# Optimization experiments

Hardware: AMD Instinct MI355X
Metric: run time of the kernel (lower is better)

## Reference

```python
import jax, jax.numpy as jnp
import numpy as np

N_NODES = 10000
N_EDGES = 160000
C_IN = 64      # in_irreps = 64x0e
C_TP = 16      # in_tp_irreps = 16x0e
C_KEY = 8      # key_irreps = (mul//2) = 8x0e
C_SH = 4       # spherical_harmonics_irreps = 4x0e
C_OTP = 16     # out_tp_irreps = 16x0e
C_OUT = 64     # out_irreps = 64x0e
EF = 32        # n_edge_features
FC = 128       # fc_dim (hardcoded in module)
W_NUMEL_K = C_TP * C_SH * C_KEY   # 512
W_NUMEL_V = C_TP * C_SH * C_OTP   # 1024
EPS = 1e-5


def _mlp(x, W1, b1, W2, b2, W3, b3):
    h = jax.nn.relu(x @ W1 + b1)
    h = jax.nn.relu(h @ W2 + b2)
    return h @ W3 + b3


def setup_inputs() -> dict:
    key = jax.random.key(0)
    ks = jax.random.split(key, 24)
    def nrm(k, shape, scale=1.0):
        return jax.random.normal(k, shape, dtype=jnp.float32) * scale
    inp = {}
    inp["node_data"] = nrm(ks[0], (N_NODES, C_IN))
    inp["edge_index"] = jax.random.randint(ks[1], (2, N_EDGES), 0, N_NODES, dtype=jnp.int32)
    inp["edge_data"] = nrm(ks[2], (N_EDGES, EF))
    inp["edge_sh"] = nrm(ks[3], (N_EDGES, C_SH))
    # e3nn Linear / TP internal weights (scalar-irrep specialization)
    inp["W_input"] = nrm(ks[4], (C_IN, C_TP))
    inp["W_query"] = nrm(ks[5], (C_TP, C_KEY))
    inp["W_dot"] = nrm(ks[6], (C_KEY, C_KEY))
    inp["W_output"] = nrm(ks[7], (C_OTP, C_OUT))
    # fc_key MLP: EF -> FC -> FC -> W_NUMEL_K
    inp["Wk1"] = nrm(ks[8], (EF, FC), 1.0 / np.sqrt(EF)); inp["bk1"] = jnp.zeros((FC,), jnp.float32)
    inp["Wk2"] = nrm(ks[9], (FC, FC), 1.0 / np.sqrt(FC)); inp["bk2"] = jnp.zeros((FC,), jnp.float32)
    inp["Wk3"] = nrm(ks[10], (FC, W_NUMEL_K), 1.0 / np.sqrt(FC)); inp["bk3"] = jnp.zeros((W_NUMEL_K,), jnp.float32)
    # fc_value MLP: EF -> FC -> FC -> W_NUMEL_V
    inp["Wv1"] = nrm(ks[11], (EF, FC), 1.0 / np.sqrt(EF)); inp["bv1"] = jnp.zeros((FC,), jnp.float32)
    inp["Wv2"] = nrm(ks[12], (FC, FC), 1.0 / np.sqrt(FC)); inp["bv2"] = jnp.zeros((FC,), jnp.float32)
    inp["Wv3"] = nrm(ks[13], (FC, W_NUMEL_V), 1.0 / np.sqrt(FC)); inp["bv3"] = jnp.zeros((W_NUMEL_V,), jnp.float32)
    inp["bn_weight"] = jnp.ones((C_OUT,), jnp.float32)
    inp["bn_bias"] = jnp.zeros((C_OUT,), jnp.float32)
    return inp


def reference(node_data, edge_index, edge_data, edge_sh,
              W_input, W_query, W_dot, W_output,
              Wk1, bk1, Wk2, bk2, Wk3, bk3,
              Wv1, bv1, Wv2, bv2, Wv3, bv3,
              bn_weight, bn_bias):
    N = node_data.shape[0]
    E = edge_data.shape[0]
    src, dst = edge_index[0], edge_index[1]

    # input_linear (e3nn Linear -> fan-in normalized matmul for scalar irreps)
    t = node_data @ W_input / np.sqrt(C_IN)          # [N, C_TP]
    q = t @ W_query / np.sqrt(C_TP)                  # [N, C_KEY]

    # dynamically generated per-edge TP weights
    wk = _mlp(edge_data, Wk1, bk1, Wk2, bk2, Wk3, bk3).reshape(E, C_TP, C_SH, C_KEY)
    wv = _mlp(edge_data, Wv1, bv1, Wv2, bv2, Wv3, bv3).reshape(E, C_TP, C_SH, C_OTP)

    ts = t[src]                                      # gather source node features [E, C_TP]
    # FullyConnectedTensorProduct on scalar irreps == per-edge weighted bilinear
    k = jnp.einsum('ea,es,easb->eb', ts, edge_sh, wk) / np.sqrt(C_TP * C_SH)   # [E, C_KEY]
    v = jnp.einsum('ea,es,easb->eb', ts, edge_sh, wv) / np.sqrt(C_TP * C_SH)   # [E, C_OTP]

    # dot(q[dest], k) -> scalar attention logit per edge
    a = (jnp.einsum('ea,eb,ab->e', q[dst], k, W_dot) / np.sqrt(C_KEY * C_KEY))[:, None]  # [E, 1]

    # segment softmax over edges grouped by destination node
    m = jax.ops.segment_max(a, dst, num_segments=N)
    m = jnp.where(jnp.isfinite(m), m, 0.0)           # empty segments -> 0 (matches scatter_max fill)
    a = jnp.exp(a - m[dst])
    z = jax.ops.segment_sum(a, dst, num_segments=N)
    a = a / z[dst]

    agg = jax.ops.segment_sum(a * v, dst, num_segments=N)   # [N, C_OTP]

    out = agg @ W_output / np.sqrt(C_OTP)            # [N, C_OUT]
    # residual: F.pad(node_data, (0, C_OUT - C_IN)); here C_OUT == C_IN so plain add
    out = out + node_data

    # e3nn BatchNorm on scalar irreps (training-mode batch stats, affine)
    mean = out.mean(axis=0)
    c = out - mean
    var = (c * c).mean(axis=0)
    out = c * jax.lax.rsqrt(var + EPS) * bn_weight + bn_bias
    return out
```

## Files before the change

kernel.cpp:

```cpp
#include <hip/hip_runtime.h>

#define N_NODES 10000
#define N_EDGES 160000

typedef unsigned short u16;
typedef unsigned int   u32;
typedef __bf16 bf16x8 __attribute__((ext_vector_type(8)));
typedef float  f32x4  __attribute__((ext_vector_type(4)));
typedef unsigned short u16x4 __attribute__((ext_vector_type(4)));

struct InP { const void* p[22]; };

static constexpr size_t WS_FLAG = 0;
static constexpr size_t WS_WIN  = 256;
static constexpr size_t WS_WQ   = WS_WIN  + 4096;
static constexpr size_t WS_WD   = WS_WQ   + 512;
static constexpr size_t WS_WOUT = WS_WD   + 256;
static constexpr size_t WS_BK1  = WS_WOUT + 4096;
static constexpr size_t WS_BK2  = WS_BK1  + 512;
static constexpr size_t WS_BK3  = WS_BK2  + 512;
static constexpr size_t WS_BV1  = WS_BK3  + 2048;
static constexpr size_t WS_BV2  = WS_BV1  + 512;
static constexpr size_t WS_BV3  = WS_BV2  + 512;
static constexpr size_t WS_BNW  = WS_BV3  + 4096;
static constexpr size_t WS_BNB  = WS_BNW  + 256;
static constexpr size_t WS_WK1T = WS_BNB  + 256;
static constexpr size_t WS_WK2T = WS_WK1T + 8192;
static constexpr size_t WS_WK3T = WS_WK2T + 32768;
static constexpr size_t WS_WV1T = WS_WK3T + 131072;
static constexpr size_t WS_WV2T = WS_WV1T + 8192;
static constexpr size_t WS_WV3T = WS_WV2T + 32768;
static constexpr size_t WS_T    = WS_WV3T + 262144;
static constexpr size_t WS_Q    = WS_T    + (size_t)N_NODES*16*4;
static constexpr size_t WS_Z    = WS_Q    + (size_t)N_NODES*8*4;
static constexpr size_t WS_AGG  = WS_Z    + (size_t)N_NODES*4;
static constexpr size_t WS_BNS  = WS_AGG  + (size_t)N_NODES*16*4;
static constexpr size_t WS_BNQ  = WS_BNS  + 256;
static constexpr size_t WS_OUTP = WS_BNQ  + 256;
static constexpr size_t ZERO_OFF = WS_Z;
static constexpr size_t ZERO_LEN = WS_OUTP - WS_Z;

__device__ __forceinline__ float loadf(const void* p, long i, int isbf){
  if(isbf){
    u32 x = ((u32)((const u16*)p)[i]) << 16;
    return __uint_as_float(x);
  }
  return ((const float*)p)[i];
}
__device__ __forceinline__ u16 f2b(float f){
  u32 u = __float_as_uint(f);
  u += 0x7fffu + ((u >> 16) & 1u);
  return (u16)(u >> 16);
}
__device__ __forceinline__ float b2f(u16 v){
  return __uint_as_float(((u32)v) << 16);
}
__device__ __forceinline__ bf16x8 ld8(const u16* p){
  uint4 v = *(const uint4*)p;
  return __builtin_bit_cast(bf16x8, v);
}

__global__ void k_detect(const void* edge_data, int* flag){
  int lane = threadIdx.x;
  u16 v = ((const u16*)edge_data)[lane*2];
  int ex = (v >> 7) & 0xFF;
  int sane = (ex >= 100 && ex <= 140) ? 1 : 0;
  unsigned long long b = __ballot(sane);
  if(lane == 0) flag[0] = (__popcll(b) >= 48) ? 1 : 0;
}

__global__ void k_convert(InP in, char* ws){
  const int isbf = *(const int*)(ws + WS_FLAG);
  long idx = (long)blockIdx.x*256 + threadIdx.x;
  const int    fsrc[12] = {4,5,6,7,9,11,13,15,17,19,20,21};
  const int    fcnt[12] = {1024,128,64,1024,128,128,512,128,128,1024,64,64};
  const size_t fdst[12] = {WS_WIN,WS_WQ,WS_WD,WS_WOUT,WS_BK1,WS_BK2,WS_BK3,WS_BV1,WS_BV2,WS_BV3,WS_BNW,WS_BNB};
  const long F_TOTAL = 4416;
  if(idx < F_TOTAL){
    long g = idx;
    for(int s=0;s<12;s++){
      if(g < fcnt[s]){ ((float*)(ws+fdst[s]))[g] = loadf(in.p[fsrc[s]], g, isbf); return; }
      g -= fcnt[s];
    }
    return;
  }
  long g = idx - F_TOTAL;
  const int    tsrc[6] = {8,10,12,14,16,18};
  const int    tK[6]   = {32,128,128,32,128,128};
  const int    tN[6]   = {128,128,512,128,128,1024};
  const size_t tdst[6] = {WS_WK1T,WS_WK2T,WS_WK3T,WS_WV1T,WS_WV2T,WS_WV3T};
  for(int s=0;s<6;s++){
    long cnt = (long)tK[s]*tN[s];
    if(g < cnt){
      int nk = tK[s] >> 5;
      int i = (int)(g & 7), ln = (int)((g>>3) & 63);
      int r2 = (int)(g >> 9);
      int kk = r2 % nk; int r3 = r2 / nk;
      int nt = r3 & 1;  int c  = r3 >> 1;
      int n = c*32 + nt*16 + (ln & 15);
      int k = kk*32 + (ln >> 4)*8 + i;
      ((u16*)(ws+tdst[s]))[g] = f2b(loadf(in.p[tsrc[s]], (long)k*tN[s] + n, isbf));
      return;
    }
    g -= cnt;
  }
}

__global__ void k_tq(InP in, char* ws){
  const int isbf = *(const int*)(ws + WS_FLAG);
  __shared__ float sWin[1024];
  __shared__ float sWq[128];
  __shared__ float sN[1024];
  __shared__ float sT[256];
  float* t_ws = (float*)(ws+WS_T);
  float* q_ws = (float*)(ws+WS_Q);
  int tid = threadIdx.x;
  for(int i=tid;i<1024;i+=256) sWin[i] = ((const float*)(ws+WS_WIN))[i];
  if(tid<128) sWq[tid] = ((const float*)(ws+WS_WQ))[tid];
  int n0 = blockIdx.x*16;
  for(int i=tid;i<1024;i+=256) sN[i] = loadf(in.p[0], (long)n0*64 + i, isbf);
  __syncthreads();
  int ni = tid>>4, j = tid&15;
  float acc = 0.f;
  #pragma unroll 8
  for(int i=0;i<64;i++) acc += sN[ni*64+i]*sWin[i*16+j];
  float t = acc*0.125f;
  t_ws[(n0+ni)*16+j] = t;
  sT[tid] = t;
  __syncthreads();
  if(tid<128){
    int n2 = tid>>3, b = tid&7;
    float a2 = 0.f;
    #pragma unroll
    for(int jj=0;jj<16;jj++) a2 += sT[n2*16+jj]*sWq[jj*8+b];
    q_ws[(n0+n2)*8+b] = a2*0.25f;
  }
}

__global__ __launch_bounds__(256,3) void k_edges(InP in, char* ws){
  const int isbf = *(const int*)(ws + WS_FLAG);
  const int* ei = (const int*)in.p[1];
  const float* t_ws = (const float*)(ws + WS_T);
  const float* q_ws = (const float*)(ws + WS_Q);
  float* Zp  = (float*)(ws + WS_Z);
  float* AGG = (float*)(ws + WS_AGG);

  __shared__ __align__(16) char smem[51200];
  u16*   sED = (u16*)smem;
  u16*   sH1 = (u16*)(smem + 4096);
  u16*   sH2 = (u16*)(smem + 20480);
  u16*   sPT = (u16*)(smem + 36864);
  float* sK  = (float*)(smem + 45056);
  float* sV  = (float*)(smem + 47104);
  float* sP  = (float*)smem;
  int*   sDst= (int*)(smem + 256);

  const int tid  = threadIdx.x;
  const int e0   = blockIdx.x * 64;
  const int lane = tid & 63, wv = tid >> 6;
  const int lrow = lane & 15, lquad = lane >> 4;

  {
    int e = tid >> 2, q4 = tid & 3;
    u16 tmp[8];
    if(isbf){
      uint4 vv = *(const uint4*)((const u16*)in.p[2] + (long)(e0+e)*32 + q4*8);
      *(uint4*)tmp = vv;
    } else {
      const float* fp = (const float*)in.p[2] + (long)(e0+e)*32 + q4*8;
      f32x4 a = *(const f32x4*)fp, b = *(const f32x4*)(fp+4);
      #pragma unroll
      for(int r=0;r<4;r++){ tmp[r]=f2b(a[r]); tmp[4+r]=f2b(b[r]); }
    }
    *(uint4*)&sED[(e>>4)*512 + (q4*16 + (e&15))*8] = *(uint4*)tmp;
  }
  {
    int e = tid >> 2, j4 = tid & 3;
    int src = ei[e0+e];
    *(f32x4*)&sV[e*16 + j4*4] = *(const f32x4*)&t_ws[src*16 + j4*4];
  }
  {
    int e = tid >> 2, s4 = tid & 3;
    sK[tid] = loadf(in.p[3], (long)(e0+e)*4 + s4, isbf);
  }
  float qreg[8]; int mydst = 0;
  if(wv == 0){
    mydst = ei[N_EDGES + e0 + lane];
    #pragma unroll
    for(int a=0;a<8;a++) qreg[a] = q_ws[mydst*8 + a];
  }
  __syncthreads();
  for(int idx = tid; idx < 4096; idx += 256){
    int e = idx & 63, as = idx >> 6;
    sPT[as*64 + e] = f2b(sV[e*16 + (as>>2)] * sK[e*4 + (as&3)]);
  }
  __syncthreads();
  for(int idx = tid; idx < 1536; idx += 256) sK[idx] = 0.f;

  auto dense = [&](const u16* A, int ts, int nkL, const u16* Wg, const float* biasg, u16* O){
    bf16x8 bw[2][4]; f32x4 bb[2];
    for(int nt=0;nt<2;nt++){
      for(int kk=0;kk<nkL;kk++)
        bw[nt][kk] = ld8(&Wg[(((wv*2+nt)*nkL + kk)<<9) + lane*8]);
      bb[nt] = *(const f32x4*)&biasg[wv*32 + nt*16 + lquad*4];
    }
    for(int et=0;et<4;et++){
      bf16x8 af[4];
      for(int kk=0;kk<nkL;kk++) af[kk] = ld8(&A[et*ts + (kk<<9) + lane*8]);
      for(int nt=0;nt<2;nt++){
        f32x4 c = {0.f,0.f,0.f,0.f};
        for(int kk=0;kk<nkL;kk++)
          c = __builtin_amdgcn_mfma_f32_16x16x32_bf16(bw[nt][kk], af[kk], c, 0, 0, 0);
        u16x4 pk;
        #pragma unroll
        for(int r=0;r<4;r++){
          float h = c[r] + bb[nt][r];
          h = h > 0.f ? h : 0.f;
          pk[r] = f2b(h);
        }
        int off = et*2048 + (wv<<9) + (nt*2 + (lquad>>1))*128 + lrow*8 + (lquad&1)*4;
        *(u16x4*)&O[off] = pk;
      }
    }
  };

  auto matvec = [&](const u16* Wg, const float* biasg, int NJ, int isval){
    float kp[16];
    #pragma unroll
    for(int i=0;i<16;i++) kp[i]=0.f;
    const int c0 = wv*NJ;
    bf16x8 bw[2][2][4]; f32x4 bb[2][2];
    #pragma unroll
    for(int nt=0;nt<2;nt++){
      #pragma unroll
      for(int kk=0;kk<4;kk++)
        bw[0][nt][kk] = ld8(&Wg[(((c0*2+nt)*4 + kk)<<9) + lane*8]);
      bb[0][nt] = *(const f32x4*)&biasg[c0*32 + nt*16 + lquad*4];
    }
    #pragma unroll
    for(int j=0;j<NJ;j++){
      int cur = j&1, nxt = cur^1;
      if(j+1 < NJ){
        int cn = c0 + j + 1;
        #pragma unroll
        for(int nt=0;nt<2;nt++){
          #pragma unroll
          for(int kk=0;kk<4;kk++)
            bw[nxt][nt][kk] = ld8(&Wg[(((cn*2+nt)*4 + kk)<<9) + lane*8]);
          bb[nxt][nt] = *(const f32x4*)&biasg[cn*32 + nt*16 + lquad*4];
        }
      }
      for(int et=0;et<4;et++){
        bf16x8 af[4];
        #pragma unroll
        for(int kk=0;kk<4;kk++)
          af[kk] = ld8(&sH2[et*2048 + (kk<<9) + lane*8]);
        const int e = et*16 + lrow;
        for(int nt=0;nt<2;nt++){
          f32x4 c = {0.f,0.f,0.f,0.f};
          #pragma unroll
          for(int kk=0;kk<4;kk++)
            c = __builtin_amdgcn_mfma_f32_16x16x32_bf16(bw[cur][nt][kk], af[kk], c, 0, 0, 0);
          int n0 = (c0+j)*32 + nt*16 + lquad*4;
          int as = isval ? (n0>>4) : (n0>>3);
          float pv = b2f(sPT[as*64 + e]);
          #pragma unroll
          for(int r=0;r<4;r++)
            kp[et*4+r] += pv * (c[r] + bb[cur][nt][r]);
        }
      }
    }
    if(isval){
      for(int et=0;et<4;et++){
        int e = et*16 + lrow;
        #pragma unroll
        for(int r=0;r<4;r++)
          atomicAdd(&sV[e*16 + lquad*4 + r], kp[et*4+r]*0.125f);
      }
    } else {
      int b0 = (lquad & 1)*4;
      for(int et=0;et<4;et++){
        int e = et*16 + lrow;
        #pragma unroll
        for(int r=0;r<4;r++)
          atomicAdd(&sK[e*8 + b0 + r], kp[et*4+r]*0.125f);
      }
    }
  };

  dense(sED, 512, 1, (const u16*)(ws+WS_WK1T), (const float*)(ws+WS_BK1), sH1); __syncthreads();
  dense(sH1, 2048,4, (const u16*)(ws+WS_WK2T), (const float*)(ws+WS_BK2), sH2); __syncthreads();
  matvec((const u16*)(ws+WS_WK3T), (const float*)(ws+WS_BK3), 4, 0);
  dense(sED, 512, 1, (const u16*)(ws+WS_WV1T), (const float*)(ws+WS_BV1), sH1); __syncthreads();
  dense(sH1, 2048,4, (const u16*)(ws+WS_WV2T), (const float*)(ws+WS_BV2), sH2); __syncthreads();
  matvec((const u16*)(ws+WS_WV3T), (const float*)(ws+WS_BV3), 8, 1);            __syncthreads();

  if(wv == 0){
    const float* wdf = (const float*)(ws + WS_WD);
    float acc = 0.f;
    #pragma unroll
    for(int a=0;a<8;a++){
      float qa = qreg[a];
      #pragma unroll
      for(int b=0;b<8;b++)
        acc += qa * wdf[a*8+b] * sK[lane*8+b];
    }
    float p = __expf(acc * 0.125f);
    atomicAdd(Zp + mydst, p);
    sP[lane] = p;
    sDst[lane] = mydst;
  }
  __syncthreads();
  for(int idx = tid; idx < 1024; idx += 256){
    int e = idx >> 4;
    atomicAdd(AGG + (long)sDst[e]*16 + (idx & 15), sP[e]*sV[idx]);
  }
}

__global__ void k7a(InP in, char* ws){
  const int isbf = *(const int*)(ws + WS_FLAG);
  __shared__ float sWo[1024];
  __shared__ float ls[256], lq[256];
  int tid = threadIdx.x;
  for(int i=tid;i<1024;i+=256) sWo[i] = ((const float*)(ws+WS_WOUT))[i];
  __syncthreads();
  const float* AGG = (const float*)(ws+WS_AGG);
  const float* Zp  = (const float*)(ws+WS_Z);
  float* OUTP = (float*)(ws+WS_OUTP);
  int c = tid & 63, r4 = tid >> 6;
  float s=0.f, q=0.f;
  for(int it=0; it<20; it++){
    int n = blockIdx.x*80 + it*4 + r4;
    float z = Zp[n];
    float inv = z > 0.f ? 0.25f/z : 0.f;
    const float* ag = AGG + (long)n*16;
    float acc = 0.f;
    #pragma unroll
    for(int j=0;j<16;j++) acc += ag[j]*sWo[j*64+c];
    float o = acc*inv + loadf(in.p[0], (long)n*64 + c, isbf);
    OUTP[(long)n*64+c] = o;
    s += o; q += o*o;
  }
  ls[tid]=s; lq[tid]=q;
  __syncthreads();
  if(tid < 64){
    float ss = ls[tid]+ls[tid+64]+ls[tid+128]+ls[tid+192];
    float qq = lq[tid]+lq[tid+64]+lq[tid+128]+lq[tid+192];
    atomicAdd((float*)(ws+WS_BNS)+tid, ss);
    atomicAdd((float*)(ws+WS_BNQ)+tid, qq);
  }
}

__global__ void k7c(char* ws, void* d_out){
  const int isbf = *(const int*)(ws + WS_FLAG);
  int idx = blockIdx.x*256 + threadIdx.x;
  if(idx >= N_NODES*64) return;
  int c = idx & 63;
  float s  = ((const float*)(ws+WS_BNS))[c];
  float qq = ((const float*)(ws+WS_BNQ))[c];
  float mean = s * (1.f/N_NODES);
  float var  = qq * (1.f/N_NODES) - mean*mean;
  float sc = rsqrtf(var + 1e-5f) * ((const float*)(ws+WS_BNW))[c];
  float val = (((const float*)(ws+WS_OUTP))[idx] - mean)*sc + ((const float*)(ws+WS_BNB))[c];
  if(isbf) ((u16*)d_out)[idx] = f2b(val);
  else     ((float*)d_out)[idx] = val;
}

extern "C" void kernel_launch(void* const* d_in, const int* in_sizes, int n_in,
                              void* d_out, int out_size, void* d_ws, size_t ws_size,
                              hipStream_t stream){
  InP in;
  for(int i=0;i<22;i++) in.p[i] = d_in[i];
  char* ws = (char*)d_ws;

  hipMemsetAsync(ws + ZERO_OFF, 0, ZERO_LEN, stream);
  k_detect<<<1,64,0,stream>>>((const void*)d_in[2], (int*)(ws+WS_FLAG));
  k_convert<<<946,256,0,stream>>>(in, ws);
  k_tq<<<625,256,0,stream>>>(in, ws);
  k_edges<<<2500,256,0,stream>>>(in, ws);
  k7a<<<125,256,0,stream>>>(in, ws);
  k7c<<<2500,256,0,stream>>>(ws, d_out);
}
```

Before: 321.9 us.

## Merge prep kernels, fold edge-weight contraction into MFMA epilogue, shrink LDS

The detect, convert and node-projection kernels become one preprocessing launch. Each kernel now detects bf16 inputs inline, and small vectors are read straight from the inputs. In the edge kernel, the per-edge tensor-product weights are no longer staged as a bf16 outer-product buffer. The third MLP layer's output is contracted with the ts/sh values directly in registers, with the weight columns permuted to match, and reduced across lanes with shuffles instead of shared-memory atomics. Shared memory shrinks so occupancy can rise to 4 blocks per CU, and the node-output kernel gets twice as many blocks. This adds more cross-lane shuffles and repeated detection work in every block, and the new weight permutation is a correctness risk.

```diff
diff --git a/kernel.cpp b/kernel.cpp
--- a/kernel.cpp
+++ b/kernel.cpp
@@ -11,26 +11,15 @@
 
 struct InP { const void* p[22]; };
 
-static constexpr size_t WS_FLAG = 0;
-static constexpr size_t WS_WIN  = 256;
-static constexpr size_t WS_WQ   = WS_WIN  + 4096;
-static constexpr size_t WS_WD   = WS_WQ   + 512;
-static constexpr size_t WS_WOUT = WS_WD   + 256;
-static constexpr size_t WS_BK1  = WS_WOUT + 4096;
-static constexpr size_t WS_BK2  = WS_BK1  + 512;
-static constexpr size_t WS_BK3  = WS_BK2  + 512;
-static constexpr size_t WS_BV1  = WS_BK3  + 2048;
-static constexpr size_t WS_BV2  = WS_BV1  + 512;
-static constexpr size_t WS_BV3  = WS_BV2  + 512;
-static constexpr size_t WS_BNW  = WS_BV3  + 4096;
-static constexpr size_t WS_BNB  = WS_BNW  + 256;
-static constexpr size_t WS_WK1T = WS_BNB  + 256;
+static constexpr size_t WS_WK1T = 0;
 static constexpr size_t WS_WK2T = WS_WK1T + 8192;
 static constexpr size_t WS_WK3T = WS_WK2T + 32768;
 static constexpr size_t WS_WV1T = WS_WK3T + 131072;
 static constexpr size_t WS_WV2T = WS_WV1T + 8192;
 static constexpr size_t WS_WV3T = WS_WV2T + 32768;
-static constexpr size_t WS_T    = WS_WV3T + 262144;
+static constexpr size_t WS_BK3P = WS_WV3T + 262144;
+static constexpr size_t WS_BV3P = WS_BK3P + 2048;
+static constexpr size_t WS_T    = WS_BV3P + 4096;
 static constexpr size_t WS_Q    = WS_T    + (size_t)N_NODES*16*4;
 static constexpr size_t WS_Z    = WS_Q    + (size_t)N_NODES*8*4;
 static constexpr size_t WS_AGG  = WS_Z    + (size_t)N_NODES*4;
@@ -40,6 +29,13 @@
 static constexpr size_t ZERO_OFF = WS_Z;
 static constexpr size_t ZERO_LEN = WS_OUTP - WS_Z;
 
+__device__ __forceinline__ int detect_isbf(const void* ed){
+  int lane = threadIdx.x & 63;
+  u16 v = ((const u16*)ed)[lane*2];
+  int ex = (v >> 7) & 0xFF;
+  unsigned long long b = __ballot(ex >= 100 && ex <= 140);
+  return __popcll(b) >= 48;
+}
 __device__ __forceinline__ float loadf(const void* p, long i, int isbf){
   if(isbf){
     u32 x = ((u32)((const u16*)p)[i]) << 16;
@@ -47,6 +43,16 @@
   }
   return ((const float*)p)[i];
 }
+__device__ __forceinline__ f32x4 loadf4(const void* p, long i, int isbf){
+  if(isbf){
+    u16x4 v = *(const u16x4*)((const u16*)p + i);
+    f32x4 r;
+    #pragma unroll
+    for(int k=0;k<4;k++) r[k] = __uint_as_float(((u32)v[k])<<16);
+    return r;
+  }
+  return *(const f32x4*)((const float*)p + i);
+}
 __device__ __forceinline__ u16 f2b(float f){
   u32 u = __float_as_uint(f);
   u += 0x7fffu + ((u >> 16) & 1u);
@@ -60,54 +66,48 @@
   return __builtin_bit_cast(bf16x8, v);
 }
 
-__global__ void k_detect(const void* edge_data, int* flag){
-  int lane = threadIdx.x;
-  u16 v = ((const u16*)edge_data)[lane*2];
-  int ex = (v >> 7) & 0xFF;
-  int sane = (ex >= 100 && ex <= 140) ? 1 : 0;
-  unsigned long long b = __ballot(sane);
-  if(lane == 0) flag[0] = (__popcll(b) >= 48) ? 1 : 0;
-}
-
-__global__ void k_convert(InP in, char* ws){
-  const int isbf = *(const int*)(ws + WS_FLAG);
-  long idx = (long)blockIdx.x*256 + threadIdx.x;
-  const int    fsrc[12] = {4,5,6,7,9,11,13,15,17,19,20,21};
-  const int    fcnt[12] = {1024,128,64,1024,128,128,512,128,128,1024,64,64};
-  const size_t fdst[12] = {WS_WIN,WS_WQ,WS_WD,WS_WOUT,WS_BK1,WS_BK2,WS_BK3,WS_BV1,WS_BV2,WS_BV3,WS_BNW,WS_BNB};
-  const long F_TOTAL = 4416;
-  if(idx < F_TOTAL){
+__global__ void k_pre(InP in, char* ws){
+  const int isbf = detect_isbf(in.p[2]);
+  int bi = blockIdx.x;
+  if(bi < 934){
+    long idx = (long)bi*256 + threadIdx.x;
+    const int    cnt[6]  = {4096,16384,65536,4096,16384,131072};
+    const int    nkA[6]  = {1,4,4,1,4,4};
+    const int    tNA[6]  = {128,128,512,128,128,1024};
+    const int    srcA[6] = {8,10,12,14,16,18};
+    const int    kindA[6]= {0,0,1,0,0,2};
+    const size_t dstA[6] = {WS_WK1T,WS_WK2T,WS_WK3T,WS_WV1T,WS_WV2T,WS_WV3T};
     long g = idx;
-    for(int s=0;s<12;s++){
-      if(g < fcnt[s]){ ((float*)(ws+fdst[s]))[g] = loadf(in.p[fsrc[s]], g, isbf); return; }
-      g -= fcnt[s];
+    for(int s=0;s<6;s++){
+      if(g < cnt[s]){
+        int nk = nkA[s], tN = tNA[s], kind = kindA[s];
+        int i = (int)(g & 7), l = (int)((g>>3) & 63);
+        int r2 = (int)(g >> 9);
+        int kk = r2 % nk, c16 = r2 / nk;
+        int pc = c16*16 + (l & 15);
+        int k  = kk*32 + (l >> 4)*8 + i;
+        int j;
+        if(kind == 0) j = pc;
+        else if(kind == 1){ int w = pc>>7, lc = pc&127;
+          j = (lc>>3)*32 + (((lc>>2)&1)*2 + ((lc>>1)&1))*8 + w*2 + (lc&1); }
+        else { int w = pc>>8, lc = pc&255;
+          j = (lc>>4)*64 + ((lc>>2)&3)*16 + w*4 + (lc&3); }
+        ((u16*)(ws+dstA[s]))[g] = f2b(loadf(in.p[srcA[s]], (long)k*tN + j, isbf));
+        return;
+      }
+      g -= cnt[s];
+    }
+    if(g < 512){
+      int pc = (int)g; int w = pc>>7, lc = pc&127;
+      int j = (lc>>3)*32 + (((lc>>2)&1)*2 + ((lc>>1)&1))*8 + w*2 + (lc&1);
+      ((float*)(ws+WS_BK3P))[pc] = loadf(in.p[13], j, isbf);
+    } else {
+      int pc = (int)(g - 512); int w = pc>>8, lc = pc&255;
+      int j = (lc>>4)*64 + ((lc>>2)&3)*16 + w*4 + (lc&3);
+      ((float*)(ws+WS_BV3P))[pc] = loadf(in.p[19], j, isbf);
     }
     return;
   }
-  long g = idx - F_TOTAL;
-  const int    tsrc[6] = {8,10,12,14,16,18};
-  const int    tK[6]   = {32,128,128,32,128,128};
-  const int    tN[6]   = {128,128,512,128,128,1024};
-  const size_t tdst[6] = {WS_WK1T,WS_WK2T,WS_WK3T,WS_WV1T,WS_WV2T,WS_WV3T};
-  for(int s=0;s<6;s++){
-    long cnt = (long)tK[s]*tN[s];
-    if(g < cnt){
-      int nk = tK[s] >> 5;
-      int i = (int)(g & 7), ln = (int)((g>>3) & 63);
-      int r2 = (int)(g >> 9);
-      int kk = r2 % nk; int r3 = r2 / nk;
-      int nt = r3 & 1;  int c  = r3 >> 1;
-      int n = c*32 + nt*16 + (ln & 15);
-      int k = kk*32 + (ln >> 4)*8 + i;
-      ((u16*)(ws+tdst[s]))[g] = f2b(loadf(in.p[tsrc[s]], (long)k*tN[s] + n, isbf));
-      return;
-    }
-    g -= cnt;
-  }
-}
-
-__global__ void k_tq(InP in, char* ws){
-  const int isbf = *(const int*)(ws + WS_FLAG);
   __shared__ float sWin[1024];
   __shared__ float sWq[128];
   __shared__ float sN[1024];
@@ -115,9 +115,9 @@
   float* t_ws = (float*)(ws+WS_T);
   float* q_ws = (float*)(ws+WS_Q);
   int tid = threadIdx.x;
-  for(int i=tid;i<1024;i+=256) sWin[i] = ((const float*)(ws+WS_WIN))[i];
-  if(tid<128) sWq[tid] = ((const float*)(ws+WS_WQ))[tid];
-  int n0 = blockIdx.x*16;
+  for(int i=tid;i<1024;i+=256) sWin[i] = loadf(in.p[4], i, isbf);
+  if(tid<128) sWq[tid] = loadf(in.p[5], tid, isbf);
+  int n0 = (bi - 934)*16;
   for(int i=tid;i<1024;i+=256) sN[i] = loadf(in.p[0], (long)n0*64 + i, isbf);
   __syncthreads();
   int ni = tid>>4, j = tid&15;
@@ -137,23 +137,21 @@
   }
 }
 
-__global__ __launch_bounds__(256,3) void k_edges(InP in, char* ws){
-  const int isbf = *(const int*)(ws + WS_FLAG);
+__global__ __launch_bounds__(256,4) void k_edges(InP in, char* ws){
+  const int isbf = detect_isbf(in.p[2]);
   const int* ei = (const int*)in.p[1];
   const float* t_ws = (const float*)(ws + WS_T);
   const float* q_ws = (const float*)(ws + WS_Q);
   float* Zp  = (float*)(ws + WS_Z);
   float* AGG = (float*)(ws + WS_AGG);
 
-  __shared__ __align__(16) char smem[51200];
-  u16*   sED = (u16*)smem;
-  u16*   sH1 = (u16*)(smem + 4096);
-  u16*   sH2 = (u16*)(smem + 20480);
-  u16*   sPT = (u16*)(smem + 36864);
-  float* sK  = (float*)(smem + 45056);
-  float* sV  = (float*)(smem + 47104);
-  float* sP  = (float*)smem;
-  int*   sDst= (int*)(smem + 256);
+  __shared__ __align__(16) char smem[37376];
+  u16*   sTSH = (u16*)smem;
+  u16*   sH1  = (u16*)(smem + 2560);
+  u16*   sH2  = (u16*)(smem + 18944);
+  float* sK   = (float*)(smem + 35328);
+  float* sP   = (float*)(smem + 2560);
+  int*   sDst = (int*)(smem + 2560 + 256);
 
   const int tid  = threadIdx.x;
   const int e0   = blockIdx.x * 64;
@@ -161,149 +159,212 @@
   const int lrow = lane & 15, lquad = lane >> 4;
 
   {
-    int e = tid >> 2, q4 = tid & 3;
+    int e = tid >> 2, g4 = tid & 3;
+    int src = ei[e0 + e];
+    f32x4 tv = *(const f32x4*)&t_ws[src*16 + g4*4];
+    u16x4 pk;
+    #pragma unroll
+    for(int r=0;r<4;r++) pk[r] = f2b(tv[r]);
+    *(u16x4*)&sTSH[e*20 + g4*4] = pk;
+    sTSH[e*20 + 16 + g4] = f2b(loadf(in.p[3], (long)(e0+e)*4 + g4, isbf));
+  }
+
+  auto edfrag = [&](int et)->bf16x8{
+    long base = (long)(e0 + et*16 + lrow)*32 + lquad*8;
+    if(isbf) return ld8((const u16*)in.p[2] + base);
+    const float* fp = (const float*)in.p[2] + base;
+    f32x4 a = *(const f32x4*)fp, b = *(const f32x4*)(fp+4);
     u16 tmp[8];
-    if(isbf){
-      uint4 vv = *(const uint4*)((const u16*)in.p[2] + (long)(e0+e)*32 + q4*8);
-      *(uint4*)tmp = vv;
-    } else {
-      const float* fp = (const float*)in.p[2] + (long)(e0+e)*32 + q4*8;
-      f32x4 a = *(const f32x4*)fp, b = *(const f32x4*)(fp+4);
-      #pragma unroll
-      for(int r=0;r<4;r++){ tmp[r]=f2b(a[r]); tmp[4+r]=f2b(b[r]); }
-    }
-    *(uint4*)&sED[(e>>4)*512 + (q4*16 + (e&15))*8] = *(uint4*)tmp;
-  }
-  {
-    int e = tid >> 2, j4 = tid & 3;
-    int src = ei[e0+e];
-    *(f32x4*)&sV[e*16 + j4*4] = *(const f32x4*)&t_ws[src*16 + j4*4];
-  }
-  {
-    int e = tid >> 2, s4 = tid & 3;
-    sK[tid] = loadf(in.p[3], (long)(e0+e)*4 + s4, isbf);
-  }
-  float qreg[8]; int mydst = 0;
-  if(wv == 0){
-    mydst = ei[N_EDGES + e0 + lane];
-    #pragma unroll
-    for(int a=0;a<8;a++) qreg[a] = q_ws[mydst*8 + a];
-  }
-  __syncthreads();
-  for(int idx = tid; idx < 4096; idx += 256){
-    int e = idx & 63, as = idx >> 6;
-    sPT[as*64 + e] = f2b(sV[e*16 + (as>>2)] * sK[e*4 + (as&3)]);
-  }
-  __syncthreads();
-  for(int idx = tid; idx < 1536; idx += 256) sK[idx] = 0.f;
-
-  auto dense = [&](const u16* A, int ts, int nkL, const u16* Wg, const float* biasg, u16* O){
+    #pragma unroll
+    for(int r=0;r<4;r++){ tmp[r]=f2b(a[r]); tmp[4+r]=f2b(b[r]); }
+    return ld8(tmp);
+  };
+  auto hstore = [&](u16* O, int et, int nt, const f32x4& c, const f32x4& bb){
+    u16x4 pk;
+    #pragma unroll
+    for(int r=0;r<4;r++){
+      float h = c[r] + bb[r];
+      h = h > 0.f ? h : 0.f;
+      pk[r] = f2b(h);
+    }
+    int off = et*2048 + (wv<<9) + (nt*2 + (lquad>>1))*128 + lrow*8 + (lquad&1)*4;
+    *(u16x4*)&O[off] = pk;
+  };
+  auto dense1 = [&](const u16* Wg, const void* biasp, u16* O){
+    bf16x8 bw[2]; f32x4 bb[2];
+    #pragma unroll
+    for(int nt=0;nt<2;nt++){
+      bw[nt] = ld8(&Wg[(wv*2+nt)*512 + lane*8]);
+      bb[nt] = loadf4(biasp, wv*32 + nt*16 + lquad*4, isbf);
+    }
+    #pragma unroll
+    for(int et=0;et<4;et++){
+      bf16x8 af = edfrag(et);
+      #pragma unroll
+      for(int nt=0;nt<2;nt++){
+        f32x4 c = {0.f,0.f,0.f,0.f};
+        c = __builtin_amdgcn_mfma_f32_16x16x32_bf16(bw[nt], af, c, 0, 0, 0);
+        hstore(O, et, nt, c, bb[nt]);
+      }
+    }
+  };
+  auto dense2 = [&](const u16* A, const u16* Wg, const void* biasp, u16* O){
     bf16x8 bw[2][4]; f32x4 bb[2];
+    #pragma unroll
     for(int nt=0;nt<2;nt++){
-      for(int kk=0;kk<nkL;kk++)
-        bw[nt][kk] = ld8(&Wg[(((wv*2+nt)*nkL + kk)<<9) + lane*8]);
-      bb[nt] = *(const f32x4*)&biasg[wv*32 + nt*16 + lquad*4];
-    }
+      #pragma unroll
+      for(int kk=0;kk<4;kk++)
+        bw[nt][kk] = ld8(&Wg[(((wv*2+nt)*4)+kk)*512 + lane*8]);
+      bb[nt] = loadf4(biasp, wv*32 + nt*16 + lquad*4, isbf);
+    }
+    #pragma unroll
     for(int et=0;et<4;et++){
       bf16x8 af[4];
-      for(int kk=0;kk<nkL;kk++) af[kk] = ld8(&A[et*ts + (kk<<9) + lane*8]);
+      #pragma unroll
+      for(int kk=0;kk<4;kk++) af[kk] = ld8(&A[et*2048 + (kk<<9) + lane*8]);
+      #pragma unroll
       for(int nt=0;nt<2;nt++){
         f32x4 c = {0.f,0.f,0.f,0.f};
-        for(int kk=0;kk<nkL;kk++)
+        #pragma unroll
+        for(int kk=0;kk<4;kk++)
           c = __builtin_amdgcn_mfma_f32_16x16x32_bf16(bw[nt][kk], af[kk], c, 0, 0, 0);
-        u16x4 pk;
+        hstore(O, et, nt, c, bb[nt]);
+      }
+    }
+  };
+
+  dense1((const u16*)(ws+WS_WK1T), in.p[9], sH1);
+  __syncthreads();
+  dense2(sH1, (const u16*)(ws+WS_WK2T), in.p[11], sH2);
+  __syncthreads();
+
+  {
+    float kacc[8];
+    #pragma unroll
+    for(int i=0;i<8;i++) kacc[i]=0.f;
+    const u16* Wg = (const u16*)(ws+WS_WK3T);
+    const float* bp = (const float*)(ws+WS_BK3P);
+    #pragma unroll
+    for(int half=0; half<2; half++){
+      bf16x8 af[2][4];
+      #pragma unroll
+      for(int p2=0;p2<2;p2++)
         #pragma unroll
-        for(int r=0;r<4;r++){
-          float h = c[r] + bb[nt][r];
-          h = h > 0.f ? h : 0.f;
-          pk[r] = f2b(h);
-        }
-        int off = et*2048 + (wv<<9) + (nt*2 + (lquad>>1))*128 + lrow*8 + (lquad&1)*4;
-        *(u16x4*)&O[off] = pk;
-      }
-    }
-  };
-
-  auto matvec = [&](const u16* Wg, const float* biasg, int NJ, int isval){
-    float kp[16];
-    #pragma unroll
-    for(int i=0;i<16;i++) kp[i]=0.f;
-    const int c0 = wv*NJ;
-    bf16x8 bw[2][2][4]; f32x4 bb[2][2];
-    #pragma unroll
-    for(int nt=0;nt<2;nt++){
+        for(int kk=0;kk<4;kk++)
+          af[p2][kk] = ld8(&sH2[(half*2+p2)*2048 + (kk<<9) + lane*8]);
+      bf16x8 bw[2][4]; f32x4 bb[2];
       #pragma unroll
       for(int kk=0;kk<4;kk++)
-        bw[0][nt][kk] = ld8(&Wg[(((c0*2+nt)*4 + kk)<<9) + lane*8]);
-      bb[0][nt] = *(const f32x4*)&biasg[c0*32 + nt*16 + lquad*4];
-    }
-    #pragma unroll
-    for(int j=0;j<NJ;j++){
-      int cur = j&1, nxt = cur^1;
-      if(j+1 < NJ){
-        int cn = c0 + j + 1;
-        #pragma unroll
-        for(int nt=0;nt<2;nt++){
+        bw[0][kk] = ld8(&Wg[((wv*8)*4 + kk)*512 + lane*8]);
+      bb[0] = *(const f32x4*)&bp[(wv*8)*16 + lquad*4];
+      #pragma unroll
+      for(int jc=0;jc<8;jc++){
+        int cur = jc&1, nxt = cur^1;
+        if(jc+1 < 8){
+          int cn = wv*8 + jc + 1;
           #pragma unroll
           for(int kk=0;kk<4;kk++)
-            bw[nxt][nt][kk] = ld8(&Wg[(((cn*2+nt)*4 + kk)<<9) + lane*8]);
-          bb[nxt][nt] = *(const f32x4*)&biasg[cn*32 + nt*16 + lquad*4];
+            bw[nxt][kk] = ld8(&Wg[(cn*4 + kk)*512 + lane*8]);
+          bb[nxt] = *(const f32x4*)&bp[cn*16 + lquad*4];
         }
-      }
-      for(int et=0;et<4;et++){
-        bf16x8 af[4];
+        int a  = jc*2 + (lquad>>1);
+        int sb = (lquad&1)*2;
         #pragma unroll
-        for(int kk=0;kk<4;kk++)
-          af[kk] = ld8(&sH2[et*2048 + (kk<<9) + lane*8]);
-        const int e = et*16 + lrow;
-        for(int nt=0;nt<2;nt++){
+        for(int p2=0;p2<2;p2++){
+          int et = half*2 + p2;
+          int e  = et*16 + lrow;
           f32x4 c = {0.f,0.f,0.f,0.f};
           #pragma unroll
           for(int kk=0;kk<4;kk++)
-            c = __builtin_amdgcn_mfma_f32_16x16x32_bf16(bw[cur][nt][kk], af[kk], c, 0, 0, 0);
-          int n0 = (c0+j)*32 + nt*16 + lquad*4;
-          int as = isval ? (n0>>4) : (n0>>3);
-          float pv = b2f(sPT[as*64 + e]);
+            c = __builtin_amdgcn_mfma_f32_16x16x32_bf16(bw[cur][kk], af[p2][kk], c, 0, 0, 0);
+          float ts  = b2f(sTSH[e*20 + a]);
+          float pv0 = ts * b2f(sTSH[e*20 + 16 + sb]);
+          float pv1 = ts * b2f(sTSH[e*20 + 16 + sb + 1]);
+          kacc[et*2+0] += pv0*(c[0]+bb[cur][0]) + pv1*(c[2]+bb[cur][2]);
+          kacc[et*2+1] += pv0*(c[1]+bb[cur][1]) + pv1*(c[3]+bb[cur][3]);
+        }
+      }
+    }
+    #pragma unroll
+    for(int i=0;i<8;i++){
+      kacc[i] += __shfl_xor(kacc[i], 16);
+      kacc[i] += __shfl_xor(kacc[i], 32);
+    }
+    if(lquad == 0){
+      #pragma unroll
+      for(int et=0;et<4;et++){
+        sK[(et*16+lrow)*8 + wv*2 + 0] = kacc[et*2+0]*0.125f;
+        sK[(et*16+lrow)*8 + wv*2 + 1] = kacc[et*2+1]*0.125f;
+      }
+    }
+  }
+
+  dense1((const u16*)(ws+WS_WV1T), in.p[15], sH1);
+  __syncthreads();
+  dense2(sH1, (const u16*)(ws+WS_WV2T), in.p[17], sH2);
+  __syncthreads();
+
+  float vacc[16];
+  {
+    #pragma unroll
+    for(int i=0;i<16;i++) vacc[i]=0.f;
+    const u16* Wg = (const u16*)(ws+WS_WV3T);
+    const float* bp = (const float*)(ws+WS_BV3P);
+    #pragma unroll
+    for(int half=0; half<2; half++){
+      bf16x8 af[2][4];
+      #pragma unroll
+      for(int p2=0;p2<2;p2++)
+        #pragma unroll
+        for(int kk=0;kk<4;kk++)
+          af[p2][kk] = ld8(&sH2[(half*2+p2)*2048 + (kk<<9) + lane*8]);
+      bf16x8 bw[2][4]; f32x4 bb[2];
+      #pragma unroll
+      for(int kk=0;kk<4;kk++)
+        bw[0][kk] = ld8(&Wg[((wv*16)*4 + kk)*512 + lane*8]);
+      bb[0] = *(const f32x4*)&bp[(wv*16)*16 + lquad*4];
+      #pragma unroll
+      for(int jc=0;jc<16;jc++){
+        int cur = jc&1, nxt = cur^1;
+        if(jc+1 < 16){
+          int cn = wv*16 + jc + 1;
+          #pragma unroll
+          for(int kk=0;kk<4;kk++)
+            bw[nxt][kk] = ld8(&Wg[(cn*4 + kk)*512 + lane*8]);
+          bb[nxt] = *(const f32x4*)&bp[cn*16 + lquad*4];
+        }
+        #pragma unroll
+        for(int p2=0;p2<2;p2++){
+          int et = half*2 + p2;
+          int e  = et*16 + lrow;
+          f32x4 c = {0.f,0.f,0.f,0.f};
+          #pragma unroll
+          for(int kk=0;kk<4;kk++)
+            c = __builtin_amdgcn_mfma_f32_16x16x32_bf16(bw[cur][kk], af[p2][kk], c, 0, 0, 0);
+          float pv = b2f(sTSH[e*20 + jc]) * b2f(sTSH[e*20 + 16 + lquad]);
           #pragma unroll
           for(int r=0;r<4;r++)
-            kp[et*4+r] += pv * (c[r] + bb[cur][nt][r]);
+            vacc[et*4+r] += pv*(c[r]+bb[cur][r]);
         }
       }
     }
-    if(isval){
-      for(int et=0;et<4;et++){
-        int e = et*16 + lrow;
-        #pragma unroll
-        for(int r=0;r<4;r++)
-          atomicAdd(&sV[e*16 + lquad*4 + r], kp[et*4+r]*0.125f);
-      }
-    } else {
-      int b0 = (lquad & 1)*4;
-      for(int et=0;et<4;et++){
-        int e = et*16 + lrow;
-        #pragma unroll
-        for(int r=0;r<4;r++)
-          atomicAdd(&sK[e*8 + b0 + r], kp[et*4+r]*0.125f);
-      }
-    }
-  };
-
-  dense(sED, 512, 1, (const u16*)(ws+WS_WK1T), (const float*)(ws+WS_BK1), sH1); __syncthreads();
-  dense(sH1, 2048,4, (const u16*)(ws+WS_WK2T), (const float*)(ws+WS_BK2), sH2); __syncthreads();
-  matvec((const u16*)(ws+WS_WK3T), (const float*)(ws+WS_BK3), 4, 0);
-  dense(sED, 512, 1, (const u16*)(ws+WS_WV1T), (const float*)(ws+WS_BV1), sH1); __syncthreads();
-  dense(sH1, 2048,4, (const u16*)(ws+WS_WV2T), (const float*)(ws+WS_BV2), sH2); __syncthreads();
-  matvec((const u16*)(ws+WS_WV3T), (const float*)(ws+WS_BV3), 8, 1);            __syncthreads();
+    #pragma unroll
+    for(int i=0;i<16;i++){
+      vacc[i] += __shfl_xor(vacc[i], 16);
+      vacc[i] += __shfl_xor(vacc[i], 32);
+      vacc[i] *= 0.125f;
+    }
+  }
 
   if(wv == 0){
-    const float* wdf = (const float*)(ws + WS_WD);
+    int mydst = ei[N_EDGES + e0 + lane];
     float acc = 0.f;
     #pragma unroll
     for(int a=0;a<8;a++){
-      float qa = qreg[a];
+      float qa = q_ws[mydst*8 + a];
       #pragma unroll
       for(int b=0;b<8;b++)
-        acc += qa * wdf[a*8+b] * sK[lane*8+b];
+        acc += qa * loadf(in.p[6], a*8+b, isbf) * sK[lane*8+b];
     }
     float p = __expf(acc * 0.125f);
     atomicAdd(Zp + mydst, p);
@@ -311,26 +372,33 @@
     sDst[lane] = mydst;
   }
   __syncthreads();
-  for(int idx = tid; idx < 1024; idx += 256){
-    int e = idx >> 4;
-    atomicAdd(AGG + (long)sDst[e]*16 + (idx & 15), sP[e]*sV[idx]);
+  if(lquad == 0){
+    #pragma unroll
+    for(int et=0;et<4;et++){
+      int e = et*16 + lrow;
+      float p = sP[e];
+      long base = (long)sDst[e]*16 + wv*4;
+      #pragma unroll
+      for(int r=0;r<4;r++)
+        atomicAdd(AGG + base + r, p*vacc[et*4+r]);
+    }
   }
 }
 
 __global__ void k7a(InP in, char* ws){
-  const int isbf = *(const int*)(ws + WS_FLAG);
+  const int isbf = detect_isbf(in.p[2]);
   __shared__ float sWo[1024];
   __shared__ float ls[256], lq[256];
   int tid = threadIdx.x;
-  for(int i=tid;i<1024;i+=256) sWo[i] = ((const float*)(ws+WS_WOUT))[i];
+  for(int i=tid;i<1024;i+=256) sWo[i] = loadf(in.p[7], i, isbf);
   __syncthreads();
   const float* AGG = (const float*)(ws+WS_AGG);
   const float* Zp  = (const float*)(ws+WS_Z);
   float* OUTP = (float*)(ws+WS_OUTP);
   int c = tid & 63, r4 = tid >> 6;
   float s=0.f, q=0.f;
-  for(int it=0; it<20; it++){
-    int n = blockIdx.x*80 + it*4 + r4;
+  for(int it=0; it<10; it++){
+    int n = blockIdx.x*40 + it*4 + r4;
     float z = Zp[n];
     float inv = z > 0.f ? 0.25f/z : 0.f;
     const float* ag = AGG + (long)n*16;
@@ -351,8 +419,8 @@
   }
 }
 
-__global__ void k7c(char* ws, void* d_out){
-  const int isbf = *(const int*)(ws + WS_FLAG);
+__global__ void k7c(InP in, char* ws, void* d_out){
+  const int isbf = detect_isbf(in.p[2]);
   int idx = blockIdx.x*256 + threadIdx.x;
   if(idx >= N_NODES*64) return;
   int c = idx & 63;
@@ -360,8 +428,8 @@
   float qq = ((const float*)(ws+WS_BNQ))[c];
   float mean = s * (1.f/N_NODES);
   float var  = qq * (1.f/N_NODES) - mean*mean;
-  float sc = rsqrtf(var + 1e-5f) * ((const float*)(ws+WS_BNW))[c];
-  float val = (((const float*)(ws+WS_OUTP))[idx] - mean)*sc + ((const float*)(ws+WS_BNB))[c];
+  float sc = rsqrtf(var + 1e-5f) * loadf(in.p[20], c, isbf);
+  float val = (((const float*)(ws+WS_OUTP))[idx] - mean)*sc + loadf(in.p[21], c, isbf);
   if(isbf) ((u16*)d_out)[idx] = f2b(val);
   else     ((float*)d_out)[idx] = val;
 }
@@ -374,10 +442,8 @@
   char* ws = (char*)d_ws;
 
   hipMemsetAsync(ws + ZERO_OFF, 0, ZERO_LEN, stream);
-  k_detect<<<1,64,0,stream>>>((const void*)d_in[2], (int*)(ws+WS_FLAG));
-  k_convert<<<946,256,0,stream>>>(in, ws);
-  k_tq<<<625,256,0,stream>>>(in, ws);
+  k_pre<<<1559,256,0,stream>>>(in, ws);
   k_edges<<<2500,256,0,stream>>>(in, ws);
-  k7a<<<125,256,0,stream>>>(in, ws);
-  k7c<<<2500,256,0,stream>>>(ws, d_out);
-}
+  k7a<<<250,256,0,stream>>>(in, ws);
+  k7c<<<2500,256,0,stream>>>(in, ws, d_out);
+}
```

New measurement: 828.9 us. 157% more time.
